# Optimization experiments

Measured on AMD Instinct MI355X. Metric: run time of the kernel, lower is better.

Reference implementation:

```python
import jax, jax.numpy as jnp
import numpy as np

DIM_FEAT = 16
NFX, NFY = 64, 64        # freqSize
NX, NY = 512, 512        # gridSize
N_PTS = 262144           # number of query coordinates
TWO_PI = 2.0 * np.pi


def _freqs():
    # non-log branch of compute_freq()
    fx = np.concatenate([
        np.arange(0, (NFX + 1) // 2, dtype=np.float32),
        np.arange(-(NFX - 1) // 2, 0, dtype=np.float32),
    ]) / NX
    pfy = np.arange(NFY, dtype=np.float32) / NY  # half spectrum along y
    return jnp.asarray(fx), jnp.asarray(pfy)


def setup_inputs() -> dict:
    key = jax.random.key(0)
    k1, k2, k3 = jax.random.split(key, 3)
    coord = jax.random.uniform(k1, (N_PTS, 2), dtype=jnp.float32)  # in [0,1]
    params_real = 0.1 * jax.random.normal(k2, (1, DIM_FEAT, NFX, NFY), dtype=jnp.float32)
    params_imag = 0.1 * jax.random.normal(k3, (1, DIM_FEAT, NFX, NFY), dtype=jnp.float32)
    gaussion_var = jnp.asarray(0.001, dtype=jnp.float32)
    return {"coord": coord, "params_real": params_real,
            "params_imag": params_imag, "gaussion_var": gaussion_var}


def reference(coord, params_real, params_imag, gaussion_var):
    fx, fy = _freqs()                              # [NFX], [NFY]
    # Gaussian low-pass filter on k-space (compute_gaussian)
    ktraj = jnp.stack(jnp.meshgrid(fx, fy, indexing='ij'), axis=-1)  # [NFX,NFY,2]
    gauss = jnp.exp((-2.0 * (jnp.pi * ktraj) ** 2 * gaussion_var).sum(-1))  # [NFX,NFY]
    kspace = (params_real[0] + 1j * params_imag[0]) * gauss  # [C,NFX,NFY] complex64

    # coords in [0,1] -> pixel units (frequencies are already divided by grid size)
    pts = coord.reshape(-1, 2) * jnp.asarray([NX, NY], dtype=jnp.float32)  # [N,2]

    # non-uniform inverse real DFT over half spectrum (irdft2d):
    # feat[n,c] = Re( sum_{k,l} kspace[c,k,l] * w_l * e^{2pi i (fx_k x_n + fy_l y_n)} )
    # with w_0 = 1 and w_{l>0} = 2 (Hermitian half-spectrum along y)
    Bx = jnp.exp(1j * TWO_PI * pts[:, 0:1] * fx[None, :])            # [N,NFX] c64
    w = jnp.where(jnp.arange(NFY) == 0, 1.0, 2.0).astype(jnp.float32)
    By = jnp.exp(1j * TWO_PI * pts[:, 1:2] * fy[None, :]) * w        # [N,NFY] c64

    T = jnp.einsum('ckl,nl->nck', kspace, By)   # [N,C,NFX] complex64 (dominant buffer)
    feat = jnp.einsum('nck,nk->nc', T, Bx).real  # [N,C] float32
    return feat
```

## Files before the change

kernel.cpp:

```cpp
#include <hip/hip_runtime.h>
#include <math.h>


#define NPTS  262144
#define GX    128
#define GY    256
#define BETA  13.8f
#define PI_F      3.14159265358979323846f
#define TWO_PI_F  6.28318530717958647692f


__global__ void k_deconv(float* __restrict__ phit) {
    int b = blockIdx.x;
    float xi; int idx;
    if (b < 33) { xi = (float)b * (1.0f / (float)GX); idx = b; }
    else        { xi = (float)(b - 33) * (1.0f / (float)GY); idx = 64 + (b - 33); }
    const int NQ = 1024;
    const float h = 6.0f / (float)NQ;
    float sum = 0.0f;
    for (int i = threadIdx.x; i <= NQ; i += blockDim.x) {
        float z  = -3.0f + h * (float)i;
        float t  = z * (1.0f / 3.0f);
        float s2 = fmaxf(1.0f - t * t, 0.0f);
        float psi = expf(BETA * (sqrtf(s2) - 1.0f));
        float w = (i == 0 || i == NQ) ? 0.5f : 1.0f;
        sum += w * psi * cosf(TWO_PI_F * xi * z);
    }
    __shared__ float red[256];
    red[threadIdx.x] = sum;
    __syncthreads();
    for (int s = 128; s > 0; s >>= 1) {
        if ((int)threadIdx.x < s) red[threadIdx.x] += red[threadIdx.x + s];
        __syncthreads();
    }
    if (threadIdx.x == 0) phit[idx] = red[0] * h;
}

__global__ void k_ydft(const float* __restrict__ pr, const float* __restrict__ pim,
                       const float* __restrict__ gvar, const float* __restrict__ phit,
                       float2* __restrict__ T) {
    int ck = blockIdx.x;
    int kk = ck & 63;
    int k  = (kk < 32) ? kk : kk - 64;
    int ak = (k < 0) ? -k : k;
    __shared__ float2 cs[64];
    if (threadIdx.x < 64) {
        int l = threadIdx.x;
        float fx = (float)k * (1.0f / 512.0f);
        float fy = (float)l * (1.0f / 512.0f);
        float var = gvar[0];
        float gauss = expf(-2.0f * PI_F * PI_F * var * (fx * fx + fy * fy));
        float w = (l == 0) ? 1.0f : 2.0f;
        float scale = gauss * w / (phit[ak] * phit[64 + l]);
        int t = ck * 64 + l;
        cs[l] = make_float2(pr[t] * scale, pim[t] * scale);
    }
    __syncthreads();
    int Y = threadIdx.x;
    float th = TWO_PI_F * (float)Y * (1.0f / (float)GY);
    float s1, c1;
    sincosf(th, &s1, &c1);
    float cr = 1.0f, sr = 0.0f, ar = 0.0f, ai = 0.0f;
    for (int l = 0; l < 64; ++l) {
        float2 cv = cs[l];
        ar = fmaf(cv.x, cr, ar); ar = fmaf(-cv.y, sr, ar);
        ai = fmaf(cv.x, sr, ai); ai = fmaf(cv.y, cr, ai);
        float cn = fmaf(cr, c1, -sr * s1);
        float sn = fmaf(sr, c1,  cr * s1);
        cr = cn; sr = sn;
    }
    T[ck * 256 + Y] = make_float2(ar, ai);
}

__global__ void k_xdft(const float2* __restrict__ T, float* __restrict__ g) {
    int X  = blockIdx.x;
    int c0 = blockIdx.y * 4;
    int Y  = threadIdx.x;
    float th = TWO_PI_F * (float)X * (1.0f / (float)GX);
    float s1, c1;
    sincosf(th, &s1, &c1);
    float sgn = (X & 1) ? -1.0f : 1.0f;
    float cr = 1.0f, sr = 0.0f;
    float a0 = 0.f, a1 = 0.f, a2 = 0.f, a3 = 0.f;
    for (int kk = 0; kk < 64; ++kk) {
        float fr = (kk >= 32) ? cr * sgn : cr;
        float fi = (kk >= 32) ? sr * sgn : sr;
        float2 t0 = T[((c0 + 0) * 64 + kk) * 256 + Y];
        float2 t1 = T[((c0 + 1) * 64 + kk) * 256 + Y];
        float2 t2 = T[((c0 + 2) * 64 + kk) * 256 + Y];
        float2 t3 = T[((c0 + 3) * 64 + kk) * 256 + Y];
        a0 = fmaf(t0.x, fr, a0); a0 = fmaf(-t0.y, fi, a0);
        a1 = fmaf(t1.x, fr, a1); a1 = fmaf(-t1.y, fi, a1);
        a2 = fmaf(t2.x, fr, a2); a2 = fmaf(-t2.y, fi, a2);
        a3 = fmaf(t3.x, fr, a3); a3 = fmaf(-t3.y, fi, a3);
        float cn = fmaf(cr, c1, -sr * s1);
        float sn = fmaf(sr, c1,  cr * s1);
        cr = cn; sr = sn;
    }
    *(float4*)(g + ((size_t)X * 256 + (size_t)Y) * 16 + c0) = make_float4(a0, a1, a2, a3);
}

__global__ __launch_bounds__(256) void k_sample(const float2* __restrict__ coord,
                                                const float* __restrict__ g,
                                                float* __restrict__ out) {
    int n   = blockIdx.x * 32 + (threadIdx.x >> 3);
    int sub = threadIdx.x & 7;
    float2 uv = coord[n];
    float px = uv.x * (float)GX;
    float py = uv.y * (float)GY;
    int ix0 = (int)floorf(px) - 2;
    int iy0 = (int)floorf(py) - 2;
    float wx[6], wy[6];
#pragma unroll
    for (int i = 0; i < 6; ++i) {
        float zx = px - (float)(ix0 + i);
        float tx = zx * (1.0f / 3.0f);
        float sx2 = fmaxf(1.0f - tx * tx, 0.0f);
        wx[i] = __expf(BETA * (sqrtf(sx2) - 1.0f));
        float zy = py - (float)(iy0 + i);
        float ty = zy * (1.0f / 3.0f);
        float sy2 = fmaxf(1.0f - ty * ty, 0.0f);
        wy[i] = __expf(BETA * (sqrtf(sy2) - 1.0f));
    }
    int yo[6];
#pragma unroll
    for (int j = 0; j < 6; ++j)
        yo[j] = ((iy0 + j) & (GY - 1)) * 16 + sub * 2;
    float acc0 = 0.0f, acc1 = 0.0f;
#pragma unroll
    for (int i = 0; i < 6; ++i) {
        const float* rowp = g + (size_t)(((ix0 + i) & (GX - 1)) * (GY * 16));
        float wxi = wx[i];
#pragma unroll
        for (int j = 0; j < 6; ++j) {
            float2 v = *(const float2*)(rowp + yo[j]);
            float w = wxi * wy[j];
            acc0 = fmaf(w, v.x, acc0);
            acc1 = fmaf(w, v.y, acc1);
        }
    }
    *(float2*)(out + (size_t)n * 16 + sub * 2) = make_float2(acc0, acc1);
}

extern "C" void kernel_launch(void* const* d_in, const int* in_sizes, int n_in,
                              void* d_out, int out_size, void* d_ws, size_t ws_size,
                              hipStream_t stream) {
    const float* coord = (const float*)d_in[0];
    const float* preal = (const float*)d_in[1];
    const float* pimag = (const float*)d_in[2];
    const float* gvar  = (const float*)d_in[3];

    char*   ws   = (char*)d_ws;
    float*  phit = (float*)(ws + 0);
    float2* T    = (float2*)(ws + 1048576);
    float*  g    = (float*)(ws + 3145728);
    float*  out  = (float*)d_out;

    hipLaunchKernelGGL(k_deconv, dim3(97),          dim3(256), 0, stream, phit);
    hipLaunchKernelGGL(k_ydft,   dim3(1024),        dim3(256), 0, stream, preal, pimag, gvar, phit, T);
    hipLaunchKernelGGL(k_xdft,   dim3(128, 4),      dim3(256), 0, stream, T, g);
    hipLaunchKernelGGL(k_sample, dim3(NPTS/32),     dim3(256), 0, stream, (const float2*)coord, g, out);
}
```

Measured before the change: 126.3 us.

## Store oversampled grid in fp16 and shrink NUFFT kernel to width 5

Changes the Kaiser-Bessel interpolation kernel from width 6 to width 5, adjusting beta and the deconvolution quadrature to match. The intermediate grid is now stored as fp16, which halves its footprint. The sampling kernel has each thread handle 4 channels with 8-byte loads, and each block covers 64 points. These changes cut gather bandwidth and the tap count from 36 to 25 per point, at the cost of lower interpolation accuracy and fp16 rounding of grid values.

Result: faster. 106.7 us (-15.5%).

```diff
diff --git a/kernel.cpp b/kernel.cpp
--- a/kernel.cpp
+++ b/kernel.cpp
@@ -1,11 +1,12 @@
 #include <hip/hip_runtime.h>
+#include <hip/hip_fp16.h>
 #include <math.h>
 
 
 #define NPTS  262144
 #define GX    128
 #define GY    256
-#define BETA  13.8f
+#define BETA  11.5f
 #define PI_F      3.14159265358979323846f
 #define TWO_PI_F  6.28318530717958647692f
 
@@ -16,11 +17,11 @@
     if (b < 33) { xi = (float)b * (1.0f / (float)GX); idx = b; }
     else        { xi = (float)(b - 33) * (1.0f / (float)GY); idx = 64 + (b - 33); }
     const int NQ = 1024;
-    const float h = 6.0f / (float)NQ;
+    const float h = 5.0f / (float)NQ;
     float sum = 0.0f;
     for (int i = threadIdx.x; i <= NQ; i += blockDim.x) {
-        float z  = -3.0f + h * (float)i;
-        float t  = z * (1.0f / 3.0f);
+        float z  = -2.5f + h * (float)i;
+        float t  = z * 0.4f;
         float s2 = fmaxf(1.0f - t * t, 0.0f);
         float psi = expf(BETA * (sqrtf(s2) - 1.0f));
         float w = (i == 0 || i == NQ) ? 0.5f : 1.0f;
@@ -72,7 +73,7 @@
     T[ck * 256 + Y] = make_float2(ar, ai);
 }
 
-__global__ void k_xdft(const float2* __restrict__ T, float* __restrict__ g) {
+__global__ void k_xdft(const float2* __restrict__ T, __half* __restrict__ gh) {
     int X  = blockIdx.x;
     int c0 = blockIdx.y * 4;
     int Y  = threadIdx.x;
@@ -97,49 +98,58 @@
         float sn = fmaf(sr, c1,  cr * s1);
         cr = cn; sr = sn;
     }
-    *(float4*)(g + ((size_t)X * 256 + (size_t)Y) * 16 + c0) = make_float4(a0, a1, a2, a3);
+    union { __half2 h[2]; float2 f; } u;
+    u.h[0] = __floats2half2_rn(a0, a1);
+    u.h[1] = __floats2half2_rn(a2, a3);
+    *(float2*)((char*)gh + (size_t)X * 8192 + (size_t)Y * 32 + (size_t)c0 * 2) = u.f;
 }
 
 __global__ __launch_bounds__(256) void k_sample(const float2* __restrict__ coord,
-                                                const float* __restrict__ g,
+                                                const __half* __restrict__ gh,
                                                 float* __restrict__ out) {
-    int n   = blockIdx.x * 32 + (threadIdx.x >> 3);
-    int sub = threadIdx.x & 7;
+    int n   = blockIdx.x * 64 + (threadIdx.x >> 2);
+    int sub = threadIdx.x & 3;
     float2 uv = coord[n];
     float px = uv.x * (float)GX;
     float py = uv.y * (float)GY;
-    int ix0 = (int)floorf(px) - 2;
-    int iy0 = (int)floorf(py) - 2;
-    float wx[6], wy[6];
+    int ix0 = (int)floorf(px + 0.5f) - 2;
+    int iy0 = (int)floorf(py + 0.5f) - 2;
+    float wx[5], wy[5];
 #pragma unroll
-    for (int i = 0; i < 6; ++i) {
+    for (int i = 0; i < 5; ++i) {
         float zx = px - (float)(ix0 + i);
-        float tx = zx * (1.0f / 3.0f);
+        float tx = zx * 0.4f;
         float sx2 = fmaxf(1.0f - tx * tx, 0.0f);
         wx[i] = __expf(BETA * (sqrtf(sx2) - 1.0f));
         float zy = py - (float)(iy0 + i);
-        float ty = zy * (1.0f / 3.0f);
+        float ty = zy * 0.4f;
         float sy2 = fmaxf(1.0f - ty * ty, 0.0f);
         wy[i] = __expf(BETA * (sqrtf(sy2) - 1.0f));
     }
-    int yo[6];
+    int yo[5];
 #pragma unroll
-    for (int j = 0; j < 6; ++j)
-        yo[j] = ((iy0 + j) & (GY - 1)) * 16 + sub * 2;
-    float acc0 = 0.0f, acc1 = 0.0f;
+    for (int j = 0; j < 5; ++j)
+        yo[j] = ((iy0 + j) & (GY - 1)) * 32 + sub * 8;
+    float a0 = 0.f, a1 = 0.f, a2 = 0.f, a3 = 0.f;
 #pragma unroll
-    for (int i = 0; i < 6; ++i) {
-        const float* rowp = g + (size_t)(((ix0 + i) & (GX - 1)) * (GY * 16));
+    for (int i = 0; i < 5; ++i) {
+        const char* rowp = (const char*)gh + (size_t)(((ix0 + i) & (GX - 1)) * 8192);
         float wxi = wx[i];
 #pragma unroll
-        for (int j = 0; j < 6; ++j) {
-            float2 v = *(const float2*)(rowp + yo[j]);
+        for (int j = 0; j < 5; ++j) {
+            float2 raw = *(const float2*)(rowp + yo[j]);
+            __half2 h01 = *reinterpret_cast<const __half2*>(&raw.x);
+            __half2 h23 = *reinterpret_cast<const __half2*>(&raw.y);
+            float2 v01 = __half22float2(h01);
+            float2 v23 = __half22float2(h23);
             float w = wxi * wy[j];
-            acc0 = fmaf(w, v.x, acc0);
-            acc1 = fmaf(w, v.y, acc1);
+            a0 = fmaf(w, v01.x, a0);
+            a1 = fmaf(w, v01.y, a1);
+            a2 = fmaf(w, v23.x, a2);
+            a3 = fmaf(w, v23.y, a3);
         }
     }
-    *(float2*)(out + (size_t)n * 16 + sub * 2) = make_float2(acc0, acc1);
+    *(float4*)(out + (size_t)n * 16 + sub * 4) = make_float4(a0, a1, a2, a3);
 }
 
 extern "C" void kernel_launch(void* const* d_in, const int* in_sizes, int n_in,
@@ -153,11 +163,11 @@
     char*   ws   = (char*)d_ws;
     float*  phit = (float*)(ws + 0);
     float2* T    = (float2*)(ws + 1048576);
-    float*  g    = (float*)(ws + 3145728);
+    __half* gh   = (__half*)(ws + 3145728);
     float*  out  = (float*)d_out;
 
     hipLaunchKernelGGL(k_deconv, dim3(97),          dim3(256), 0, stream, phit);
     hipLaunchKernelGGL(k_ydft,   dim3(1024),        dim3(256), 0, stream, preal, pimag, gvar, phit, T);
-    hipLaunchKernelGGL(k_xdft,   dim3(128, 4),      dim3(256), 0, stream, T, g);
-    hipLaunchKernelGGL(k_sample, dim3(NPTS/32),     dim3(256), 0, stream, (const float2*)coord, g, out);
+    hipLaunchKernelGGL(k_xdft,   dim3(128, 4),      dim3(256), 0, stream, T, gh);
+    hipLaunchKernelGGL(k_sample, dim3(NPTS/64),     dim3(256), 0, stream, (const float2*)coord, gh, out);
 }
```
